# Optimization experiments

Hardware: AMD Instinct MI355X
Metric: run time of the kernel (lower is better)

Reference implementation:

```python
import jax, jax.numpy as jnp
import numpy as np

B, C, D, H, W = 2, 180, 16, 32, 32
NH, WS, I = 6, 8, 2
HD = C // NH
SCALE = HD ** -0.5
N = WS ** 3                      # 512 tokens per window
TABLE = (2 * WS - 1) ** 3        # 3375 relative-position entries
HID = int(C * 4.0)               # MLP hidden
CR = C // 3                      # CAB compressed channels (compress_ratio=3)
SQ = C // 30                     # channel-attn squeeze (squeeze_factor=30)
CONV_SCALE = 0.01
EPS = 1e-5


def layer_norm(x, g, b):
    m = jnp.mean(x, axis=-1, keepdims=True)
    v = jnp.mean((x - m) ** 2, axis=-1, keepdims=True)
    return (x - m) * jax.lax.rsqrt(v + EPS) * g + b


def setup_inputs() -> dict:
    key = jax.random.key(0)
    ks = jax.random.split(key, 12)
    n = lambda i, shape: jax.random.normal(ks[i], shape, jnp.float32) * 0.02
    return {
        "x": jax.random.normal(ks[0], (B, D * H * W, C), jnp.float32),
        "x_size_d": D, "x_size_h": H, "x_size_w": W,
        "rpi_sa": jax.random.randint(ks[1], (N, N), 0, TABLE),
        "attn_mask": jnp.zeros((1,), jnp.float32),
        "triangular_masks": jnp.zeros((1,), jnp.float32),
        "g1": jnp.ones((C,), jnp.float32), "b1": jnp.zeros((C,), jnp.float32),
        "qkv_w": n(2, (3 * C, C)), "qkv_b": jnp.zeros((3 * C,), jnp.float32),
        "rpb": n(3, (TABLE, NH)),
        "proj_w": n(4, (C, C)), "proj_b": jnp.zeros((C,), jnp.float32),
        "cw1": n(5, (CR, C, 3, 3, 3)), "cb1": jnp.zeros((CR,), jnp.float32),
        "cw2": n(6, (C, CR, 3, 3, 3)), "cb2": jnp.zeros((C,), jnp.float32),
        "caw1": n(7, (SQ, C)), "cab1": jnp.zeros((SQ,), jnp.float32),
        "caw2": n(8, (C, SQ)), "cab2": jnp.zeros((C,), jnp.float32),
        "g2": jnp.ones((C,), jnp.float32), "b2": jnp.zeros((C,), jnp.float32),
        "fc1_w": n(9, (HID, C)), "fc1_b": jnp.zeros((HID,), jnp.float32),
        "fc2_w": n(10, (C, HID)), "fc2_b": jnp.zeros((C,), jnp.float32),
    }


def reference(x, x_size_d, x_size_h, x_size_w, rpi_sa, attn_mask, triangular_masks,
              g1, b1, qkv_w, qkv_b, rpb, proj_w, proj_b,
              cw1, cb1, cw2, cb2, caw1, cab1, caw2, cab2,
              g2, b2, fc1_w, fc1_b, fc2_w, fc2_b):
    Dd, Hd, Wd = x_size_d, x_size_h, x_size_w
    shortcut = x
    xn = layer_norm(x, g1, b1).reshape(B, Dd, Hd, Wd, C)

    # ---- CAB conv branch (conv3 -> gelu -> conv3 -> channel attention) ----
    xc = jnp.transpose(xn, (0, 4, 1, 2, 3))  # B C D H W
    dn = ("NCDHW", "OIDHW", "NCDHW")
    y = jax.lax.conv_general_dilated(xc, cw1, (1, 1, 1), "SAME", dimension_numbers=dn)
    y = jax.nn.gelu(y + cb1[None, :, None, None, None], approximate=False)
    y = jax.lax.conv_general_dilated(y, cw2, (1, 1, 1), "SAME", dimension_numbers=dn)
    y = y + cb2[None, :, None, None, None]
    pooled = jnp.mean(y, axis=(2, 3, 4))                      # B C (AdaptiveAvgPool3d(1))
    a = jax.nn.relu(pooled @ caw1.T + cab1)
    a = jax.nn.sigmoid(a @ caw2.T + cab2)                     # B C
    y = y * a[:, :, None, None, None]
    conv_x = jnp.transpose(y, (0, 2, 3, 4, 1)).reshape(B, Dd * Hd * Wd, C)

    # ---- sparse interval partition (interval=2, no pad, no shift) ----
    Gd, Gh, Gw = Dd // I, Hd // I, Wd // I
    xs = xn.reshape(B, Gd, I, Gh, I, Gw, I, C)
    xs = jnp.transpose(xs, (0, 2, 4, 6, 1, 3, 5, 7)).reshape(B * I ** 3, Gd, Gh, Gw, C)

    # ---- 3D window partition ----
    nd, nh, nw = Gd // WS, Gh // WS, Gw // WS
    xw = xs.reshape(-1, nd, WS, nh, WS, nw, WS, C)
    xw = jnp.transpose(xw, (0, 1, 3, 5, 2, 4, 6, 7)).reshape(-1, N, C)

    # ---- window attention with relative-position bias ----
    qkv = (xw @ qkv_w.T + qkv_b).reshape(-1, N, 3, NH, HD)
    qkv = jnp.transpose(qkv, (2, 0, 3, 1, 4))                 # 3, nWin, NH, N, HD
    q, k, v = qkv[0] * SCALE, qkv[1], qkv[2]
    attn = jnp.einsum("whnd,whmd->whnm", q, k)
    bias = rpb[rpi_sa.reshape(-1)].reshape(N, N, NH)
    attn = jax.nn.softmax(attn + jnp.transpose(bias, (2, 0, 1))[None], axis=-1)
    out = jnp.einsum("whnm,whmd->whnd", attn, v)
    out = jnp.transpose(out, (0, 2, 1, 3)).reshape(-1, N, C)
    out = out @ proj_w.T + proj_b

    # ---- window reverse + sparse reverse ----
    xs = out.reshape(-1, nd, nh, nw, WS, WS, WS, C)
    xs = jnp.transpose(xs, (0, 1, 4, 2, 5, 3, 6, 7)).reshape(B * I ** 3, Gd, Gh, Gw, C)
    xs = xs.reshape(B, I, I, I, Gd, Gh, Gw, C)
    xs = jnp.transpose(xs, (0, 4, 1, 5, 2, 6, 3, 7)).reshape(B, Dd, Hd, Wd, C)
    attn_x = xs.reshape(B, Dd * Hd * Wd, C)

    # ---- residual + conv branch, then MLP ----
    x = shortcut + attn_x + conv_x * CONV_SCALE
    h = layer_norm(x, g2, b2)
    h = jax.nn.gelu(h @ fc1_w.T + fc1_b, approximate=False) @ fc2_w.T + fc2_b
    return x + h
```

## Files before the change

kernel.cpp:

```cpp
#include <hip/hip_runtime.h>
#include <math.h>

static constexpr int CCH = 180;
static constexpr float SCALE_Q = 0.18257418583505536f;

typedef short short8 __attribute__((ext_vector_type(8)));
typedef float f32x4 __attribute__((ext_vector_type(4)));

static constexpr size_t OFF_ATTNB = 0;
static constexpr size_t OFF_XNB   = 3145728;
static constexpr size_t OFF_Y1B   = 6291456;
static constexpr size_t OFF_QKVB  = 7340032;
static constexpr size_t OFF_HID   = 0;
static constexpr size_t OFF_Y2B   = 16777216;
static constexpr size_t OFF_X2    = 19922944;
static constexpr size_t OFF_X2N   = 25821184;
static constexpr size_t OFF_BIASB = 28966912;
static constexpr size_t OFF_WQKV  = 29753344;
static constexpr size_t OFF_WPROJ = 29814784;
static constexpr size_t OFF_WFC1  = 29839360;
static constexpr size_t OFF_WFC2  = 29913088;
static constexpr size_t OFF_WB1   = 30011392;
static constexpr size_t OFF_WB2   = 30177280;
static constexpr size_t OFF_PPART = 30343168;
static constexpr size_t OFF_POOL  = 30354688;
static constexpr size_t OFF_AM    = 30355048;

__device__ __forceinline__ float geluf(float v){
  return 0.5f*v*(1.0f + erff(v*0.70710678118654752440f));
}
__device__ __forceinline__ short f2bf(float f){
  unsigned u = __float_as_uint(f);
  unsigned r = (u + 0x7FFFu + ((u>>16)&1u)) >> 16;
  return (short)r;
}
__device__ __forceinline__ float bf2f(short s){
  return __uint_as_float(((unsigned)(unsigned short)s)<<16);
}
__device__ __forceinline__ void gload16(const void* g, void* l){
  __builtin_amdgcn_global_load_lds(
    (const __attribute__((address_space(1))) unsigned int*)g,
    (__attribute__((address_space(3))) unsigned int*)l, 16, 0, 0);
}

__global__ void prep_wb(const float* __restrict__ qkv_w, const float* __restrict__ proj_w,
                        const float* __restrict__ fc1_w, const float* __restrict__ fc2_w,
                        short* __restrict__ wq, short* __restrict__ wp,
                        short* __restrict__ w1, short* __restrict__ w2){
  int i = blockIdx.x*256 + threadIdx.x;
  if(i < 122880){
    int o = i/192, k = i - o*192;
    wq[i] = (o<540 && k<180) ? f2bf(qkv_w[o*180+k]) : (short)0;
  } else if(i < 172032){
    int j = i-122880; int o = j/192, k = j - o*192;
    wp[j] = (o<180 && k<180) ? f2bf(proj_w[o*180+k]) : (short)0;
  } else if(i < 319488){
    int j = i-172032; int o = j/192, k = j - o*192;
    w1[j] = (o<720 && k<180) ? f2bf(fc1_w[o*180+k]) : (short)0;
  } else if(i < 516096){
    int j = i-319488; int o = j/768, k = j - o*768;
    w2[j] = (o<180 && k<720) ? f2bf(fc2_w[o*720+k]) : (short)0;
  }
}

__global__ void prep_wbc(const float* __restrict__ cw1, const float* __restrict__ cw2,
                         short* __restrict__ wb1, short* __restrict__ wb2){
  int i = blockIdx.x*256 + threadIdx.x;
  if(i < 27*64*192){
    int t = i/(64*192); int rem = i - t*64*192;
    int co = rem/192, ci = rem - co*192;
    wb1[i] = (co<60 && ci<180) ? f2bf(cw1[(co*180+ci)*27 + t]) : (short)0;
    int co2 = rem/64, ci2 = rem - co2*64;
    wb2[i] = (co2<180 && ci2<60) ? f2bf(cw2[(co2*60+ci2)*27 + t]) : (short)0;
  }
}

__global__ __launch_bounds__(256) void bias_prep(const int* __restrict__ rpi,
    const float* __restrict__ rpb, short* __restrict__ biasB){
  int i = blockIdx.x*256 + threadIdx.x;
  int q = i>>9, k = i&511;
  int kt = k>>5, kin = k&31;
  int j = kt*32 + ((kin<16) ? 2*kin : 2*(kin-16)+1);
  int idx = rpi[i];
  #pragma unroll
  for(int h=0;h<6;h++)
    biasB[((size_t)h*512 + q)*512 + j] = f2bf(rpb[idx*6+h]);
}

__global__ __launch_bounds__(256) void ln_bf16(const float* __restrict__ x,
    const float* __restrict__ g, const float* __restrict__ b, short* __restrict__ outb){
  int token = blockIdx.x*4 + (threadIdx.x>>6);
  int lane  = threadIdx.x & 63;
  const float* row = x + (size_t)token*CCH;
  float v0 = row[lane], v1 = row[lane+64];
  float v2 = (lane<52) ? row[lane+128] : 0.f;
  float s = v0+v1+v2;
  #pragma unroll
  for(int m=1;m<64;m<<=1) s += __shfl_xor(s, m, 64);
  float mean = s*(1.f/180.f);
  float d0=v0-mean, d1=v1-mean, d2=(lane<52)?(v2-mean):0.f;
  float sq = d0*d0+d1*d1+d2*d2;
  #pragma unroll
  for(int m=1;m<64;m<<=1) sq += __shfl_xor(sq, m, 64);
  float rstd = rsqrtf(sq*(1.f/180.f)+1e-5f);
  short* o = outb + (size_t)token*192;
  o[lane]    = f2bf(d0*rstd*g[lane]    + b[lane]);
  o[lane+64] = f2bf(d1*rstd*g[lane+64] + b[lane+64]);
  o[lane+128]= (lane<52) ? f2bf(d2*rstd*g[lane+128] + b[lane+128]) : (short)0;
}

__global__ __launch_bounds__(256) void conv1_mfma(const short* __restrict__ in,
    const short* __restrict__ wb, const float* __restrict__ cbias, short* __restrict__ y1b){
  __shared__ short lds[136*192];
  int bid = blockIdx.x;
  int xcd = bid&7, idx = bid>>3;
  int b = idx>>5, dd = (idx>>4)&1, hg = idx&15;
  int d = xcd*2+dd;
  int h0 = hg*2;
  int tid = threadIdx.x, l=tid&63, l15=l&15, g=l>>4, wid=tid>>6;
  int hrow = wid&1, coh = wid>>1;
  f32x4 acc[2][2];
  #pragma unroll
  for(int mi=0;mi<2;mi++)
    #pragma unroll
    for(int nj=0;nj<2;nj++) acc[mi][nj]=(f32x4){0.f,0.f,0.f,0.f};
  short8 stg[13];

  auto LOADS = [&](int kd){
    int dp = d+kd-1;
    bool dok = (unsigned)dp<16u;
    const short* src = in + ((size_t)(b*16 + (dok?dp:0))*1024)*192;
    #pragma unroll
    for(int it=0; it<13; it++){
      if(it<12 || tid<192){
        int idx2 = tid + it*256;
        int rr = idx2/24, s = idx2 - rr*24;
        int hl = rr/34, wl = rr - hl*34;
        int hh = h0 - 1 + hl, w = wl - 1;
        short8 v = (short8){0,0,0,0,0,0,0,0};
        if(dok && (unsigned)hh<32u && (unsigned)w<32u)
          v = *(const short8*)&src[((size_t)hh*32+w)*192 + s*8];
        stg[it] = v;
      }
    }
  };
  auto WRITES = [&](){
    #pragma unroll
    for(int it=0; it<13; it++){
      if(it<12 || tid<192){
        int idx2 = tid + it*256;
        int rr = idx2/24, s = idx2 - rr*24;
        *(short8*)&lds[rr*192 + (((s&~7)|((s&7)^(rr&7)))<<3)] = stg[it];
      }
    }
  };
  LOADS(0); WRITES(); __syncthreads();
  for(int kd=0; kd<3; kd++){
    if(kd<2) LOADS(kd+1);
    #pragma unroll
    for(int kh=0;kh<3;kh++)
    #pragma unroll
    for(int kw=0;kw<3;kw++){
      const short* wt = wb + (size_t)((kd*3+kh)*3+kw)*12288;
      #pragma unroll
      for(int ks=0;ks<6;ks++){
        int s = ks*4+g;
        short8 av[2], bv[2];
        #pragma unroll
        for(int mi=0;mi<2;mi++){
          int rr = (hrow+kh)*34 + kw + mi*16 + l15;
          av[mi] = *(const short8*)&lds[rr*192 + (((s&~7)|((s&7)^(rr&7)))<<3)];
        }
        #pragma unroll
        for(int nj=0;nj<2;nj++)
          bv[nj] = *(const short8*)&wt[(size_t)(coh*32+nj*16+l15)*192 + ks*32 + g*8];
        #pragma unroll
        for(int mi=0;mi<2;mi++)
          #pragma unroll
          for(int nj=0;nj<2;nj++)
            acc[mi][nj] = __builtin_amdgcn_mfma_f32_16x16x32_bf16(av[mi], bv[nj], acc[mi][nj],0,0,0);
      }
    }
    __syncthreads();
    if(kd<2){ WRITES(); __syncthreads(); }
  }
  size_t token0 = ((size_t)(b*16+d)*32 + h0)*32;
  #pragma unroll
  for(int mi=0;mi<2;mi++)
    #pragma unroll
    for(int nj=0;nj<2;nj++){
      int co = coh*32 + nj*16 + l15;
      float bb = (co<60)? cbias[co] : 0.f;
      #pragma unroll
      for(int reg=0;reg<4;reg++){
        int r = hrow*32 + mi*16 + g*4 + reg;
        y1b[(token0 + r)*64 + co] = f2bf(geluf(acc[mi][nj][reg] + bb));
      }
    }
}

__global__ __launch_bounds__(512) void conv2_mfma(const short* __restrict__ in,
    const short* __restrict__ wb, const float* __restrict__ cbias, short* __restrict__ y2b){
  __shared__ short lds[136*64];
  int bid = blockIdx.x;
  int xcd = bid&7, idx = bid>>3;
  int b = idx>>5, dd = (idx>>4)&1, hg = idx&15;
  int d = xcd*2+dd;
  int h0 = hg*2;
  int tid = threadIdx.x, l=tid&63, l15=l&15, g=l>>4, wid=tid>>6;
  int hrow = wid&1, coq = wid>>1;
  f32x4 acc[2][3];
  #pragma unroll
  for(int mi=0;mi<2;mi++)
    #pragma unroll
    for(int nj=0;nj<3;nj++) acc[mi][nj]=(f32x4){0.f,0.f,0.f,0.f};
  short8 stg[3];

  auto LOADS = [&](int kd){
    int dp = d+kd-1;
    bool dok = (unsigned)dp<16u;
    const short* src = in + ((size_t)(b*16 + (dok?dp:0))*1024)*64;
    #pragma unroll
    for(int it=0; it<3; it++){
      if(it<2 || tid<64){
        int idx2 = tid + it*512;
        int rr = idx2>>3, s = idx2&7;
        int hl = rr/34, wl = rr - hl*34;
        int hh = h0 - 1 + hl, w = wl - 1;
        short8 v = (short8){0,0,0,0,0,0,0,0};
        if(dok && (unsigned)hh<32u && (unsigned)w<32u)
          v = *(const short8*)&src[((size_t)hh*32+w)*64 + s*8];
        stg[it] = v;
      }
    }
  };
  auto WRITES = [&](){
    #pragma unroll
    for(int it=0; it<3; it++){
      if(it<2 || tid<64){
        int idx2 = tid + it*512;
        int rr = idx2>>3, s = idx2&7;
        *(short8*)&lds[rr*64 + ((s^(rr&7))<<3)] = stg[it];
      }
    }
  };
  LOADS(0); WRITES(); __syncthreads();
  for(int kd=0; kd<3; kd++){
    if(kd<2) LOADS(kd+1);
    #pragma unroll
    for(int kh=0;kh<3;kh++)
    #pragma unroll
    for(int kw=0;kw<3;kw++){
      const short* wt = wb + (size_t)((kd*3+kh)*3+kw)*12288;
      #pragma unroll
      for(int ks=0;ks<2;ks++){
        int s = ks*4+g;
        short8 av[2], bv[3];
        #pragma unroll
        for(int mi=0;mi<2;mi++){
          int rr = (hrow+kh)*34 + kw + mi*16 + l15;
          av[mi] = *(const short8*)&lds[rr*64 + ((s^(rr&7))<<3)];
        }
        #pragma unroll
        for(int nj=0;nj<3;nj++)
          bv[nj] = *(const short8*)&wt[(size_t)(coq*48+nj*16+l15)*64 + ks*32 + g*8];
        #pragma unroll
        for(int mi=0;mi<2;mi++)
          #pragma unroll
          for(int nj=0;nj<3;nj++)
            acc[mi][nj] = __builtin_amdgcn_mfma_f32_16x16x32_bf16(av[mi], bv[nj], acc[mi][nj],0,0,0);
      }
    }
    __syncthreads();
    if(kd<2){ WRITES(); __syncthreads(); }
  }
  size_t token0 = ((size_t)(b*16+d)*32 + h0)*32;
  #pragma unroll
  for(int mi=0;mi<2;mi++)
    #pragma unroll
    for(int nj=0;nj<3;nj++){
      int co = coq*48 + nj*16 + l15;
      float bb = (co<180)? cbias[co] : 0.f;
      #pragma unroll
      for(int reg=0;reg<4;reg++){
        int r = hrow*32 + mi*16 + g*4 + reg;
        y2b[(token0 + r)*192 + co] = f2bf(acc[mi][nj][reg] + bb);
      }
    }
}

__global__ __launch_bounds__(192) void pool1_kernel(const short* __restrict__ y2b,
                                                    float* __restrict__ part){
  int b = blockIdx.x>>5, chunk = blockIdx.x&31;
  int c = threadIdx.x;
  if(c<180){
    float s = 0.f;
    const short* base = y2b + ((size_t)b*16384 + chunk*512)*192 + c;
    for(int it=0;it<512;it++) s += bf2f(base[(size_t)it*192]);
    part[blockIdx.x*180 + c] = s;
  }
}
__global__ void pool2_kernel(const float* __restrict__ part, float* __restrict__ pooled){
  int i = blockIdx.x*256 + threadIdx.x;
  if(i<360){
    int b = i/180, c = i - b*180;
    float s = 0.f;
    for(int ch=0;ch<32;ch++) s += part[(b*32+ch)*180 + c];
    pooled[i] = s*(1.f/16384.f);
  }
}

__global__ void chattn_kernel(const float* __restrict__ pooled,
    const float* __restrict__ caw1, const float* __restrict__ cab1,
    const float* __restrict__ caw2, const float* __restrict__ cab2,
    float* __restrict__ amask){
  __shared__ float hid[2][6];
  int t = threadIdx.x;
  if(t<12){
    int b = t/6, qh = t - b*6;
    float s = cab1[qh];
    for(int c=0;c<180;c++) s += pooled[b*180+c]*caw1[qh*180+c];
    hid[b][qh] = fmaxf(s, 0.f);
  }
  __syncthreads();
  for(int i=t;i<360;i+=64){
    int b = i/180, c = i - b*180;
    float s = cab2[c];
    #pragma unroll
    for(int qh=0;qh<6;qh++) s += hid[b][qh]*caw2[c*6+qh];
    amask[i] = 1.f/(1.f+__expf(-s));
  }
}

__device__ __forceinline__ int wtok_to_row(int t){
  int win = t >> 9, n = t & 511;
  int sb = win >> 2, wi = win & 3;
  int wh = wi >> 1, ww = wi & 1;
  int b  = sb >> 3, r = sb & 7;
  int id = r >> 2, ih = (r>>1)&1, iw = r&1;
  int td = n >> 6, th = (n>>3)&7, tw = n & 7;
  int dd = td*2 + id;
  int hh = (wh*8+th)*2 + ih;
  int wwp= (ww*8+tw)*2 + iw;
  return b*16384 + (dd*32+hh)*32 + wwp;
}

template<int MODE, int NOUT, int KTOT>
__global__ __launch_bounds__(256) void mgemm(const short* __restrict__ A,
    const short* __restrict__ Wb, const float* __restrict__ bias, void* __restrict__ outv,
    const float* __restrict__ e0, const float* __restrict__ e1,
    const float* __restrict__ e2){
  __shared__ short As[2][8192];
  __shared__ short Bs[2][8192];
  __shared__ int rowmap[128];
  int lin = blockIdx.y*gridDim.x + blockIdx.x;
  int xcd = lin&7, k = lin>>3;
  int bm = xcd*32 + (k & 31);
  int bn = k >> 5;
  int tid = threadIdx.x;
  int l = tid&63, l15=l&15, g=l>>4, wid=tid>>6;
  int wm = wid>>1, wn = wid&1;
  constexpr int RS = (MODE==3)?768:192;
  if(MODE==0 || MODE==1){
    if(tid<128) rowmap[tid] = wtok_to_row(bm*128+tid);
  }
  __syncthreads();
  f32x4 acc[4][4];
  #pragma unroll
  for(int i=0;i<4;i++)
    #pragma unroll
    for(int j=0;j<4;j++) acc[i][j] = (f32x4){0.f,0.f,0.f,0.f};

  constexpr int NCH = KTOT/64;
  auto STAGE = [&](int ch, int p){
    int k0 = ch*64;
    #pragma unroll
    for(int it=0; it<4; it++){
      int i = it*256 + wid*64 + l;
      int r = i>>3, sl = (i&7) ^ (r&7);
      size_t row = (MODE==0) ? (size_t)rowmap[r] : (size_t)(bm*128+r);
      gload16(A + row*RS + k0 + sl*8, &As[p][(size_t)(it*256+wid*64)*8]);
    }
    #pragma unroll
    for(int it=0; it<4; it++){
      int i = it*256 + wid*64 + l;
      int c = i>>3, sl = (i&7) ^ (c&7);
      gload16(Wb + (size_t)(bn*128+c)*KTOT + k0 + sl*8, &Bs[p][(size_t)(it*256+wid*64)*8]);
    }
  };
  STAGE(0,0);
  for(int ch=0; ch<NCH; ch++){
    if(ch+1<NCH){
      STAGE(ch+1,(ch+1)&1);
      asm volatile("s_waitcnt vmcnt(8)" ::: "memory");
    } else {
      asm volatile("s_waitcnt vmcnt(0)" ::: "memory");
    }
    __builtin_amdgcn_s_barrier();
    const short* as = As[ch&1];
    const short* bs = Bs[ch&1];
    #pragma unroll
    for(int ks=0; ks<2; ks++){
      short8 av[4], bv[4];
      #pragma unroll
      for(int i=0;i<4;i++){
        int r = wm*64 + i*16 + l15;
        av[i] = *(const short8*)&as[r*64 + (((ks*4+g) ^ (r&7))<<3)];
      }
      #pragma unroll
      for(int j=0;j<4;j++){
        int c = wn*64 + j*16 + l15;
        bv[j] = *(const short8*)&bs[c*64 + (((ks*4+g) ^ (c&7))<<3)];
      }
      #pragma unroll
      for(int i=0;i<4;i++)
        #pragma unroll
        for(int j=0;j<4;j++)
          acc[i][j] = __builtin_amdgcn_mfma_f32_16x16x32_bf16(av[i], bv[j], acc[i][j],0,0,0);
    }
    asm volatile("" ::: "memory");
    __builtin_amdgcn_s_barrier();
  }
  #pragma unroll
  for(int i=0;i<4;i++){
    int rloc0 = wm*64 + i*16 + g*4;
    #pragma unroll
    for(int j=0;j<4;j++){
      int o = bn*128 + wn*64 + j*16 + l15;
      if(MODE!=2 && o>=NOUT) continue;
      float bb = (o<NOUT) ? bias[o] : 0.f;
      #pragma unroll
      for(int reg=0; reg<4; reg++){
        int rl = rloc0 + reg;
        int trow = bm*128 + rl;
        float v = acc[i][j][reg] + bb;
        if(MODE==0){
          int which = o/180; int chn = o - which*180;
          int head = chn/30; int hd = chn - head*30;
          int win = trow>>9, n = trow&511;
          if(which==0){
            size_t sidx = ((size_t)(win*6+head)*512 + n)*32;
            ((short*)outv)[sidx + hd] = f2bf(v*SCALE_Q);
            if(hd==0) *(int*)&((short*)outv)[sidx + 30] = 0;
          } else if(which==1){
            size_t sidx = 6291456 + ((size_t)(win*6+head)*512 + n)*32;
            ((short*)outv)[sidx + hd] = f2bf(v);
            if(hd==0) *(int*)&((short*)outv)[sidx + 30] = 0;
          } else {
            ((short*)outv)[12582912 + ((size_t)(win*6+head)*32 + hd)*512 + n] = f2bf(v);
          }
        } else if(MODE==1){
          int grow = rowmap[rl];
          float conv = bf2f(((const short*)e1)[(size_t)grow*192 + o]);
          float am   = e2[(grow>>14)*180 + o];
          ((float*)outv)[(size_t)grow*180+o] = v + e0[(size_t)grow*180+o] + conv*am*0.01f;
        } else if(MODE==2){
          ((short*)outv)[(size_t)trow*768+o] = (o<720) ? f2bf(geluf(v)) : (short)0;
        } else {
          ((float*)outv)[(size_t)trow*180+o] = v + e0[(size_t)trow*180+o];
        }
      }
    }
  }
}

__global__ __launch_bounds__(256) void attn_mfma(const short* __restrict__ qkvb,
    const short* __restrict__ biasB, short* __restrict__ attnb){
  __shared__ short Ks[1024];
  __shared__ short Vt[1024];
  __shared__ short Ps[4096];
  int bid = blockIdx.x;
  int j0 = bid>>3;
  int grp = (bid&7)*48 + (j0>>2);
  int qt = j0&3;
  int win = grp/6, head = grp - (grp/6)*6;
  int tid = threadIdx.x, w = tid>>6, l = tid&63, l15 = l&15, g = l>>4;
  const short* qp = qkvb + (size_t)(win*6+head)*16384;
  const short* kp = qp + 6291456;
  const short* vp = qkvb + 12582912 + (size_t)(win*6+head)*16384;
  int qbase = qt*128 + w*32;
  short8 aq0 = *(const short8*)&qp[(size_t)(qbase + l15)*32 + g*8];
  short8 aq1 = *(const short8*)&qp[(size_t)(qbase + 16 + l15)*32 + g*8];
  const short* bB = biasB + ((size_t)head*512 + qbase)*512;
  f32x4 acc[2][2];
  float lsum[2][4];
  #pragma unroll
  for(int a=0;a<2;a++){
    #pragma unroll
    for(int r=0;r<4;r++) lsum[a][r]=0.f;
    #pragma unroll
    for(int b=0;b<2;b++) acc[a][b]=(f32x4){0.f,0.f,0.f,0.f};
  }
  int pbase = w*1024;
  int rrA = l15>>1, sA = ((l15&1)<<2)|g;
  int offT0 = rrA*64 + ((sA ^ (rrA&7))<<3);
  int rrB = 8+rrA;
  int offT1 = rrB*64 + ((sA ^ (rrB&7))<<3);
  int strr = (tid&127)>>3, sts = tid&7;
  int stoff = strr*64 + ((sts ^ (strr&7))<<3);
  int sttok = strr*2 + (sts>>2), sthd8 = (sts&3)*8;

  for(int kt=0; kt<16; kt++){
    if(tid<128){
      short8 v = *(const short8*)&kp[(size_t)(kt*32+sttok)*32 + sthd8];
      *(short8*)&Ks[stoff] = v;
    } else {
      short8 v = *(const short8*)&vp[(size_t)sttok*512 + kt*32 + sthd8];
      *(short8*)&Vt[stoff] = v;
    }
    unsigned ub[2][4];
    #pragma unroll
    for(int mf=0; mf<2; mf++)
      #pragma unroll
      for(int reg=0; reg<4; reg++)
        ub[mf][reg] = *(const unsigned*)&bB[(size_t)(mf*16+g*4+reg)*512 + kt*32 + 2*l15];
    __syncthreads();
    short8 bk0 = *(const short8*)&Ks[offT0];
    short8 bk1 = *(const short8*)&Ks[offT1];
    f32x4 z = (f32x4){0.f,0.f,0.f,0.f};
    f32x4 s00 = __builtin_amdgcn_mfma_f32_16x16x32_bf16(aq0, bk0, z,0,0,0);
    f32x4 s01 = __builtin_amdgcn_mfma_f32_16x16x32_bf16(aq0, bk1, z,0,0,0);
    f32x4 s10 = __builtin_amdgcn_mfma_f32_16x16x32_bf16(aq1, bk0, z,0,0,0);
    f32x4 s11 = __builtin_amdgcn_mfma_f32_16x16x32_bf16(aq1, bk1, z,0,0,0);
    #pragma unroll
    for(int mf=0; mf<2; mf++){
      #pragma unroll
      for(int reg=0; reg<4; reg++){
        float b0 = __uint_as_float(ub[mf][reg]<<16);
        float b1 = __uint_as_float(ub[mf][reg]&0xFFFF0000u);
        float sv0 = (mf==0)? s00[reg] : s10[reg];
        float sv1 = (mf==0)? s01[reg] : s11[reg];
        float p0 = __expf(fminf(sv0 + b0, 60.f));
        float p1 = __expf(fminf(sv1 + b1, 60.f));
        lsum[mf][reg] += p0 + p1;
        int q = mf*16 + g*4 + reg;
        int rr = q>>1;
        int s0 = ((q&1)<<2) | (l15>>3);
        int s1 = s0 + 2;
        Ps[pbase + rr*64 + ((s0 ^ (rr&7))<<3) + (l15&7)] = f2bf(p0);
        Ps[pbase + rr*64 + ((s1 ^ (rr&7))<<3) + (l15&7)] = f2bf(p1);
      }
    }
    short8 ap0 = *(const short8*)&Ps[pbase + offT0];
    short8 ap1 = *(const short8*)&Ps[pbase + offT1];
    short8 bv0 = *(const short8*)&Vt[offT0];
    short8 bv1 = *(const short8*)&Vt[offT1];
    acc[0][0] = __builtin_amdgcn_mfma_f32_16x16x32_bf16(ap0, bv0, acc[0][0],0,0,0);
    acc[0][1] = __builtin_amdgcn_mfma_f32_16x16x32_bf16(ap0, bv1, acc[0][1],0,0,0);
    acc[1][0] = __builtin_amdgcn_mfma_f32_16x16x32_bf16(ap1, bv0, acc[1][0],0,0,0);
    acc[1][1] = __builtin_amdgcn_mfma_f32_16x16x32_bf16(ap1, bv1, acc[1][1],0,0,0);
    __syncthreads();
  }
  int token = win*512 + qbase;
  #pragma unroll
  for(int mf=0; mf<2; mf++)
  #pragma unroll
  for(int reg=0; reg<4; reg++){
    float lv = lsum[mf][reg];
    lv += __shfl_xor(lv,1,64); lv += __shfl_xor(lv,2,64);
    lv += __shfl_xor(lv,4,64); lv += __shfl_xor(lv,8,64);
    float inv = 1.f/lv;
    int qg = token + mf*16 + g*4 + reg;
    short* orow = attnb + (size_t)qg*192 + head*30;
    if(l15<30) orow[l15] = f2bf(acc[mf][0][reg]*inv);
    if(l15<14) orow[16+l15] = f2bf(acc[mf][1][reg]*inv);
    if(head==5 && l15<12) attnb[(size_t)qg*192 + 180 + l15] = 0;
  }
}

extern "C" void kernel_launch(void* const* d_in, const int* in_sizes, int n_in,
                              void* d_out, int out_size, void* d_ws, size_t ws_size,
                              hipStream_t stream){
  const float* x      = (const float*)d_in[0];
  const int*   rpi    = (const int*)  d_in[4];
  const float* g1     = (const float*)d_in[7];
  const float* b1     = (const float*)d_in[8];
  const float* qkv_w  = (const float*)d_in[9];
  const float* qkv_b  = (const float*)d_in[10];
  const float* rpb    = (const float*)d_in[11];
  const float* proj_w = (const float*)d_in[12];
  const float* proj_b = (const float*)d_in[13];
  const float* cw1    = (const float*)d_in[14];
  const float* cb1    = (const float*)d_in[15];
  const float* cw2    = (const float*)d_in[16];
  const float* cb2    = (const float*)d_in[17];
  const float* caw1   = (const float*)d_in[18];
  const float* cab1   = (const float*)d_in[19];
  const float* caw2   = (const float*)d_in[20];
  const float* cab2   = (const float*)d_in[21];
  const float* g2     = (const float*)d_in[22];
  const float* b2     = (const float*)d_in[23];
  const float* fc1_w  = (const float*)d_in[24];
  const float* fc1_b  = (const float*)d_in[25];
  const float* fc2_w  = (const float*)d_in[26];
  const float* fc2_b  = (const float*)d_in[27];
  float* ws = (float*)d_ws;
  float* fout = (float*)d_out;
  short* attnb = (short*)(ws + OFF_ATTNB);
  short* xnb   = (short*)(ws + OFF_XNB);
  short* y1b   = (short*)(ws + OFF_Y1B);
  short* qkvb  = (short*)(ws + OFF_QKVB);
  short* hid   = (short*)(ws + OFF_HID);
  short* y2b   = (short*)(ws + OFF_Y2B);
  short* x2n   = (short*)(ws + OFF_X2N);
  short* biasB = (short*)(ws + OFF_BIASB);
  short* wq    = (short*)(ws + OFF_WQKV);
  short* wp    = (short*)(ws + OFF_WPROJ);
  short* w1    = (short*)(ws + OFF_WFC1);
  short* w2    = (short*)(ws + OFF_WFC2);
  short* wb1   = (short*)(ws + OFF_WB1);
  short* wb2   = (short*)(ws + OFF_WB2);

  prep_wb<<<2016,256,0,stream>>>(qkv_w, proj_w, fc1_w, fc2_w, wq, wp, w1, w2);
  prep_wbc<<<1296,256,0,stream>>>(cw1, cw2, wb1, wb2);
  bias_prep<<<1024,256,0,stream>>>(rpi, rpb, biasB);
  ln_bf16<<<8192,256,0,stream>>>(x, g1, b1, xnb);
  conv1_mfma<<<512,256,0,stream>>>(xnb, wb1, cb1, y1b);
  conv2_mfma<<<512,512,0,stream>>>(y1b, wb2, cb2, y2b);
  pool1_kernel<<<64,192,0,stream>>>(y2b, ws+OFF_PPART);
  pool2_kernel<<<2,256,0,stream>>>(ws+OFF_PPART, ws+OFF_POOL);
  chattn_kernel<<<1,64,0,stream>>>(ws+OFF_POOL, caw1, cab1, caw2, cab2, ws+OFF_AM);
  mgemm<0,540,192><<<dim3(256,5),256,0,stream>>>(
      xnb, wq, qkv_b, qkvb, nullptr, nullptr, nullptr);
  attn_mfma<<<1536,256,0,stream>>>(qkvb, biasB, attnb);
  mgemm<1,180,192><<<dim3(256,2),256,0,stream>>>(
      attnb, wp, proj_b, ws+OFF_X2, x, (const float*)y2b, ws+OFF_AM);
  ln_bf16<<<8192,256,0,stream>>>(ws+OFF_X2, g2, b2, x2n);
  mgemm<2,720,192><<<dim3(256,6),256,0,stream>>>(
      x2n, w1, fc1_b, hid, nullptr, nullptr, nullptr);
  mgemm<3,180,768><<<dim3(256,2),256,0,stream>>>(
      hid, w2, fc2_b, fout, ws+OFF_X2, nullptr, nullptr);
}
```

Before: 499.8 us.

## Use zero-padded activation layouts so conv kernels stage halos with direct LDS loads

```diff
diff --git a/kernel.cpp b/kernel.cpp
--- a/kernel.cpp
+++ b/kernel.cpp
@@ -8,23 +8,23 @@
 typedef float f32x4 __attribute__((ext_vector_type(4)));
 
 static constexpr size_t OFF_ATTNB = 0;
-static constexpr size_t OFF_XNB   = 3145728;
-static constexpr size_t OFF_Y1B   = 6291456;
-static constexpr size_t OFF_QKVB  = 7340032;
+static constexpr size_t OFF_XNP   = 3145728;
+static constexpr size_t OFF_Y1P   = 7140864;
+static constexpr size_t OFF_QKVB  = 8472576;
 static constexpr size_t OFF_HID   = 0;
-static constexpr size_t OFF_Y2B   = 16777216;
-static constexpr size_t OFF_X2    = 19922944;
-static constexpr size_t OFF_X2N   = 25821184;
-static constexpr size_t OFF_BIASB = 28966912;
-static constexpr size_t OFF_WQKV  = 29753344;
-static constexpr size_t OFF_WPROJ = 29814784;
-static constexpr size_t OFF_WFC1  = 29839360;
-static constexpr size_t OFF_WFC2  = 29913088;
-static constexpr size_t OFF_WB1   = 30011392;
-static constexpr size_t OFF_WB2   = 30177280;
-static constexpr size_t OFF_PPART = 30343168;
-static constexpr size_t OFF_POOL  = 30354688;
-static constexpr size_t OFF_AM    = 30355048;
+static constexpr size_t OFF_Y2B   = 17909760;
+static constexpr size_t OFF_X2    = 21055488;
+static constexpr size_t OFF_X2N   = 26953728;
+static constexpr size_t OFF_BIASB = 30099456;
+static constexpr size_t OFF_WQKV  = 30885888;
+static constexpr size_t OFF_WPROJ = 30947328;
+static constexpr size_t OFF_WFC1  = 30971904;
+static constexpr size_t OFF_WFC2  = 31045632;
+static constexpr size_t OFF_WB1   = 31143936;
+static constexpr size_t OFF_WB2   = 31309824;
+static constexpr size_t OFF_PPART = 31475712;
+static constexpr size_t OFF_POOL  = 31487232;
+static constexpr size_t OFF_AM    = 31487592;
 
 __device__ __forceinline__ float geluf(float v){
   return 0.5f*v*(1.0f + erff(v*0.70710678118654752440f));
@@ -87,6 +87,7 @@
     biasB[((size_t)h*512 + q)*512 + j] = f2bf(rpb[idx*6+h]);
 }
 
+template<int PADDED>
 __global__ __launch_bounds__(256) void ln_bf16(const float* __restrict__ x,
     const float* __restrict__ g, const float* __restrict__ b, short* __restrict__ outb){
   int token = blockIdx.x*4 + (threadIdx.x>>6);
@@ -103,188 +104,149 @@
   #pragma unroll
   for(int m=1;m<64;m<<=1) sq += __shfl_xor(sq, m, 64);
   float rstd = rsqrtf(sq*(1.f/180.f)+1e-5f);
-  short* o = outb + (size_t)token*192;
+  size_t orow;
+  if(PADDED){
+    int bb=token>>14, d=(token>>10)&15, h=(token>>5)&31, w=token&31;
+    orow = ((size_t)((bb*18+d+1)*34 + h+1)*34 + w+1)*192;
+  } else {
+    orow = (size_t)token*192;
+  }
+  short* o = outb + orow;
   o[lane]    = f2bf(d0*rstd*g[lane]    + b[lane]);
   o[lane+64] = f2bf(d1*rstd*g[lane+64] + b[lane+64]);
   o[lane+128]= (lane<52) ? f2bf(d2*rstd*g[lane+128] + b[lane+128]) : (short)0;
 }
 
-__global__ __launch_bounds__(256) void conv1_mfma(const short* __restrict__ in,
-    const short* __restrict__ wb, const float* __restrict__ cbias, short* __restrict__ y1b){
-  __shared__ short lds[136*192];
+__global__ __launch_bounds__(256,2) void conv1_mfma(const short* __restrict__ in,
+    const short* __restrict__ wb, const float* __restrict__ cbias, short* __restrict__ y1p){
+  __shared__ short lds[2][19584];
   int bid = blockIdx.x;
   int xcd = bid&7, idx = bid>>3;
-  int b = idx>>5, dd = (idx>>4)&1, hg = idx&15;
+  int b = idx>>6, dd=(idx>>5)&1, h=idx&31;
   int d = xcd*2+dd;
-  int h0 = hg*2;
-  int tid = threadIdx.x, l=tid&63, l15=l&15, g=l>>4, wid=tid>>6;
-  int hrow = wid&1, coh = wid>>1;
-  f32x4 acc[2][2];
+  int tid=threadIdx.x, l=tid&63, l15=l&15, g=l>>4, wid=tid>>6;
+  int soff[10];
+  #pragma unroll
+  for(int it=0; it<10; it++){
+    int i = it*256 + tid;
+    int rr = i/24, s = i - rr*24;
+    soff[it] = rr*192 + (((s&~7)|((s&7)^(rr&7)))<<3);
+  }
+  f32x4 acc[2];
+  acc[0]=(f32x4){0.f,0.f,0.f,0.f}; acc[1]=(f32x4){0.f,0.f,0.f,0.f};
+  auto STAGE=[&](int kd,int p){
+    const short* S = in + ((size_t)((b*18+d+kd)*34 + h)*34)*192;
+    #pragma unroll
+    for(int it=0; it<10; it++){
+      if(it<9 || tid<144)
+        gload16(S + soff[it], &lds[p][(it*256 + wid*64)*8]);
+    }
+  };
+  STAGE(0,0);
+  __syncthreads();
+  for(int kd=0;kd<3;kd++){
+    if(kd<2) STAGE(kd+1,(kd+1)&1);
+    const short* buf = lds[kd&1];
+    #pragma unroll
+    for(int kh=0;kh<3;kh++)
+    #pragma unroll
+    for(int kw=0;kw<3;kw++){
+      const short* wt = wb + (size_t)((kd*3+kh)*3+kw)*12288 + (wid*16+l15)*192;
+      int rr0 = kh*34+kw+l15, rr1 = rr0+16;
+      #pragma unroll
+      for(int ks=0;ks<6;ks++){
+        int s = ks*4+g;
+        short8 a0 = *(const short8*)&buf[rr0*192 + (((s&~7)|((s&7)^(rr0&7)))<<3)];
+        short8 a1 = *(const short8*)&buf[rr1*192 + (((s&~7)|((s&7)^(rr1&7)))<<3)];
+        short8 bv = *(const short8*)&wt[ks*32 + g*8];
+        acc[0] = __builtin_amdgcn_mfma_f32_16x16x32_bf16(a0, bv, acc[0],0,0,0);
+        acc[1] = __builtin_amdgcn_mfma_f32_16x16x32_bf16(a1, bv, acc[1],0,0,0);
+      }
+    }
+    __syncthreads();
+  }
+  int co = wid*16+l15;
+  float bb = (co<60)? cbias[co] : 0.f;
+  size_t row0 = ((size_t)(b*18+d+1)*34 + h+1)*34 + 1;
   #pragma unroll
   for(int mi=0;mi<2;mi++)
     #pragma unroll
-    for(int nj=0;nj<2;nj++) acc[mi][nj]=(f32x4){0.f,0.f,0.f,0.f};
-  short8 stg[13];
-
-  auto LOADS = [&](int kd){
-    int dp = d+kd-1;
-    bool dok = (unsigned)dp<16u;
-    const short* src = in + ((size_t)(b*16 + (dok?dp:0))*1024)*192;
-    #pragma unroll
-    for(int it=0; it<13; it++){
-      if(it<12 || tid<192){
-        int idx2 = tid + it*256;
-        int rr = idx2/24, s = idx2 - rr*24;
-        int hl = rr/34, wl = rr - hl*34;
-        int hh = h0 - 1 + hl, w = wl - 1;
-        short8 v = (short8){0,0,0,0,0,0,0,0};
-        if(dok && (unsigned)hh<32u && (unsigned)w<32u)
-          v = *(const short8*)&src[((size_t)hh*32+w)*192 + s*8];
-        stg[it] = v;
-      }
+    for(int reg=0;reg<4;reg++){
+      int r = mi*16 + g*4 + reg;
+      y1p[(row0 + r)*64 + co] = f2bf(geluf(acc[mi][reg] + bb));
+    }
+}
+
+__global__ __launch_bounds__(256,4) void conv2_mfma(const short* __restrict__ in,
+    const short* __restrict__ wb, const float* __restrict__ cbias, short* __restrict__ y2b){
+  __shared__ short lds[2][6528];
+  int bid = blockIdx.x;
+  int xcd = bid&7, idx = bid>>3;
+  int b = idx>>6, dd=(idx>>5)&1, h=idx&31;
+  int d = xcd*2+dd;
+  int tid=threadIdx.x, l=tid&63, l15=l&15, g=l>>4, wid=tid>>6;
+  int soff[4];
+  #pragma unroll
+  for(int it=0; it<4; it++){
+    int i = it*256 + tid;
+    int rr = i>>3, s = i&7;
+    soff[it] = rr*64 + ((s^(rr&7))<<3);
+  }
+  f32x4 acc[2][3];
+  #pragma unroll
+  for(int mi=0;mi<2;mi++)
+    #pragma unroll
+    for(int nj=0;nj<3;nj++) acc[mi][nj]=(f32x4){0.f,0.f,0.f,0.f};
+  auto STAGE=[&](int kd,int p){
+    const short* S = in + ((size_t)((b*18+d+kd)*34 + h)*34)*64;
+    #pragma unroll
+    for(int it=0; it<4; it++){
+      if(it<3 || tid<48)
+        gload16(S + soff[it], &lds[p][(it*256 + wid*64)*8]);
     }
   };
-  auto WRITES = [&](){
-    #pragma unroll
-    for(int it=0; it<13; it++){
-      if(it<12 || tid<192){
-        int idx2 = tid + it*256;
-        int rr = idx2/24, s = idx2 - rr*24;
-        *(short8*)&lds[rr*192 + (((s&~7)|((s&7)^(rr&7)))<<3)] = stg[it];
-      }
-    }
-  };
-  LOADS(0); WRITES(); __syncthreads();
-  for(int kd=0; kd<3; kd++){
-    if(kd<2) LOADS(kd+1);
+  STAGE(0,0);
+  __syncthreads();
+  for(int kd=0;kd<3;kd++){
+    if(kd<2) STAGE(kd+1,(kd+1)&1);
+    const short* buf = lds[kd&1];
     #pragma unroll
     for(int kh=0;kh<3;kh++)
     #pragma unroll
     for(int kw=0;kw<3;kw++){
       const short* wt = wb + (size_t)((kd*3+kh)*3+kw)*12288;
-      #pragma unroll
-      for(int ks=0;ks<6;ks++){
-        int s = ks*4+g;
-        short8 av[2], bv[2];
-        #pragma unroll
-        for(int mi=0;mi<2;mi++){
-          int rr = (hrow+kh)*34 + kw + mi*16 + l15;
-          av[mi] = *(const short8*)&lds[rr*192 + (((s&~7)|((s&7)^(rr&7)))<<3)];
-        }
-        #pragma unroll
-        for(int nj=0;nj<2;nj++)
-          bv[nj] = *(const short8*)&wt[(size_t)(coh*32+nj*16+l15)*192 + ks*32 + g*8];
-        #pragma unroll
-        for(int mi=0;mi<2;mi++)
-          #pragma unroll
-          for(int nj=0;nj<2;nj++)
-            acc[mi][nj] = __builtin_amdgcn_mfma_f32_16x16x32_bf16(av[mi], bv[nj], acc[mi][nj],0,0,0);
-      }
-    }
-    __syncthreads();
-    if(kd<2){ WRITES(); __syncthreads(); }
-  }
-  size_t token0 = ((size_t)(b*16+d)*32 + h0)*32;
-  #pragma unroll
-  for(int mi=0;mi<2;mi++)
-    #pragma unroll
-    for(int nj=0;nj<2;nj++){
-      int co = coh*32 + nj*16 + l15;
-      float bb = (co<60)? cbias[co] : 0.f;
-      #pragma unroll
-      for(int reg=0;reg<4;reg++){
-        int r = hrow*32 + mi*16 + g*4 + reg;
-        y1b[(token0 + r)*64 + co] = f2bf(geluf(acc[mi][nj][reg] + bb));
-      }
-    }
-}
-
-__global__ __launch_bounds__(512) void conv2_mfma(const short* __restrict__ in,
-    const short* __restrict__ wb, const float* __restrict__ cbias, short* __restrict__ y2b){
-  __shared__ short lds[136*64];
-  int bid = blockIdx.x;
-  int xcd = bid&7, idx = bid>>3;
-  int b = idx>>5, dd = (idx>>4)&1, hg = idx&15;
-  int d = xcd*2+dd;
-  int h0 = hg*2;
-  int tid = threadIdx.x, l=tid&63, l15=l&15, g=l>>4, wid=tid>>6;
-  int hrow = wid&1, coq = wid>>1;
-  f32x4 acc[2][3];
-  #pragma unroll
-  for(int mi=0;mi<2;mi++)
-    #pragma unroll
-    for(int nj=0;nj<3;nj++) acc[mi][nj]=(f32x4){0.f,0.f,0.f,0.f};
-  short8 stg[3];
-
-  auto LOADS = [&](int kd){
-    int dp = d+kd-1;
-    bool dok = (unsigned)dp<16u;
-    const short* src = in + ((size_t)(b*16 + (dok?dp:0))*1024)*64;
-    #pragma unroll
-    for(int it=0; it<3; it++){
-      if(it<2 || tid<64){
-        int idx2 = tid + it*512;
-        int rr = idx2>>3, s = idx2&7;
-        int hl = rr/34, wl = rr - hl*34;
-        int hh = h0 - 1 + hl, w = wl - 1;
-        short8 v = (short8){0,0,0,0,0,0,0,0};
-        if(dok && (unsigned)hh<32u && (unsigned)w<32u)
-          v = *(const short8*)&src[((size_t)hh*32+w)*64 + s*8];
-        stg[it] = v;
-      }
-    }
-  };
-  auto WRITES = [&](){
-    #pragma unroll
-    for(int it=0; it<3; it++){
-      if(it<2 || tid<64){
-        int idx2 = tid + it*512;
-        int rr = idx2>>3, s = idx2&7;
-        *(short8*)&lds[rr*64 + ((s^(rr&7))<<3)] = stg[it];
-      }
-    }
-  };
-  LOADS(0); WRITES(); __syncthreads();
-  for(int kd=0; kd<3; kd++){
-    if(kd<2) LOADS(kd+1);
-    #pragma unroll
-    for(int kh=0;kh<3;kh++)
-    #pragma unroll
-    for(int kw=0;kw<3;kw++){
-      const short* wt = wb + (size_t)((kd*3+kh)*3+kw)*12288;
+      int rr0 = kh*34+kw+l15, rr1 = rr0+16;
       #pragma unroll
       for(int ks=0;ks<2;ks++){
         int s = ks*4+g;
-        short8 av[2], bv[3];
-        #pragma unroll
-        for(int mi=0;mi<2;mi++){
-          int rr = (hrow+kh)*34 + kw + mi*16 + l15;
-          av[mi] = *(const short8*)&lds[rr*64 + ((s^(rr&7))<<3)];
-        }
+        short8 a0 = *(const short8*)&buf[rr0*64 + ((s^(rr0&7))<<3)];
+        short8 a1 = *(const short8*)&buf[rr1*64 + ((s^(rr1&7))<<3)];
+        short8 bv[3];
         #pragma unroll
         for(int nj=0;nj<3;nj++)
-          bv[nj] = *(const short8*)&wt[(size_t)(coq*48+nj*16+l15)*64 + ks*32 + g*8];
+          bv[nj] = *(const short8*)&wt[(size_t)(wid*48+nj*16+l15)*64 + ks*32 + g*8];
         #pragma unroll
-        for(int mi=0;mi<2;mi++)
-          #pragma unroll
-          for(int nj=0;nj<3;nj++)
-            acc[mi][nj] = __builtin_amdgcn_mfma_f32_16x16x32_bf16(av[mi], bv[nj], acc[mi][nj],0,0,0);
+        for(int nj=0;nj<3;nj++){
+          acc[0][nj] = __builtin_amdgcn_mfma_f32_16x16x32_bf16(a0, bv[nj], acc[0][nj],0,0,0);
+          acc[1][nj] = __builtin_amdgcn_mfma_f32_16x16x32_bf16(a1, bv[nj], acc[1][nj],0,0,0);
+        }
       }
     }
     __syncthreads();
-    if(kd<2){ WRITES(); __syncthreads(); }
-  }
-  size_t token0 = ((size_t)(b*16+d)*32 + h0)*32;
+  }
+  size_t token0 = ((size_t)(b*16+d)*32 + h)*32;
   #pragma unroll
   for(int mi=0;mi<2;mi++)
     #pragma unroll
     for(int nj=0;nj<3;nj++){
-      int co = coq*48 + nj*16 + l15;
-      float bb = (co<180)? cbias[co] : 0.f;
-      #pragma unroll
-      for(int reg=0;reg<4;reg++){
-        int r = hrow*32 + mi*16 + g*4 + reg;
-        y2b[(token0 + r)*192 + co] = f2bf(acc[mi][nj][reg] + bb);
+      int co = wid*48 + nj*16 + l15;
+      if(co<180){
+        float bb = cbias[co];
+        #pragma unroll
+        for(int reg=0;reg<4;reg++){
+          int r = mi*16 + g*4 + reg;
+          y2b[(token0 + r)*192 + co] = f2bf(acc[mi][nj][reg] + bb);
+        }
       }
     }
 }
@@ -332,17 +294,24 @@
   }
 }
 
-__device__ __forceinline__ int wtok_to_row(int t){
+__device__ __forceinline__ void wtok_decomp(int t, int& b, int& dd, int& hh, int& ww){
   int win = t >> 9, n = t & 511;
   int sb = win >> 2, wi = win & 3;
-  int wh = wi >> 1, ww = wi & 1;
-  int b  = sb >> 3, r = sb & 7;
+  int wh = wi >> 1, wwi = wi & 1;
+  b = sb >> 3; int r = sb & 7;
   int id = r >> 2, ih = (r>>1)&1, iw = r&1;
   int td = n >> 6, th = (n>>3)&7, tw = n & 7;
-  int dd = td*2 + id;
-  int hh = (wh*8+th)*2 + ih;
-  int wwp= (ww*8+tw)*2 + iw;
-  return b*16384 + (dd*32+hh)*32 + wwp;
+  dd = td*2 + id;
+  hh = (wh*8+th)*2 + ih;
+  ww = (wwi*8+tw)*2 + iw;
+}
+__device__ __forceinline__ int wtok_to_row(int t){
+  int b,dd,hh,ww; wtok_decomp(t,b,dd,hh,ww);
+  return b*16384 + (dd*32+hh)*32 + ww;
+}
+__device__ __forceinline__ int wtok_to_prow(int t){
+  int b,dd,hh,ww; wtok_decomp(t,b,dd,hh,ww);
+  return ((b*18+dd+1)*34 + hh+1)*34 + ww + 1;
 }
 
 template<int MODE, int NOUT, int KTOT>
@@ -362,7 +331,7 @@
   int wm = wid>>1, wn = wid&1;
   constexpr int RS = (MODE==3)?768:192;
   if(MODE==0 || MODE==1){
-    if(tid<128) rowmap[tid] = wtok_to_row(bm*128+tid);
+    if(tid<128) rowmap[tid] = (MODE==0) ? wtok_to_prow(bm*128+tid) : wtok_to_row(bm*128+tid);
   }
   __syncthreads();
   f32x4 acc[4][4];
@@ -378,7 +347,7 @@
     for(int it=0; it<4; it++){
       int i = it*256 + wid*64 + l;
       int r = i>>3, sl = (i&7) ^ (r&7);
-      size_t row = (MODE==0) ? (size_t)rowmap[r] : (size_t)(bm*128+r);
+      size_t row = (size_t)((MODE==0||MODE==1) ? rowmap[r] : bm*128+r);
       gload16(A + row*RS + k0 + sl*8, &As[p][(size_t)(it*256+wid*64)*8]);
     }
     #pragma unroll
@@ -489,7 +458,7 @@
     #pragma unroll
     for(int r=0;r<4;r++) lsum[a][r]=0.f;
     #pragma unroll
-    for(int b=0;b<2;b++) acc[a][b]=(f32x4){0.f,0.f,0.f,0.f};
+    for(int b2=0;b2<2;b2++) acc[a][b2]=(f32x4){0.f,0.f,0.f,0.f};
   }
   int pbase = w*1024;
   int rrA = l15>>1, sA = ((l15&1)<<2)|g;
@@ -597,8 +566,8 @@
   float* ws = (float*)d_ws;
   float* fout = (float*)d_out;
   short* attnb = (short*)(ws + OFF_ATTNB);
-  short* xnb   = (short*)(ws + OFF_XNB);
-  short* y1b   = (short*)(ws + OFF_Y1B);
+  short* xnp   = (short*)(ws + OFF_XNP);
+  short* y1p   = (short*)(ws + OFF_Y1P);
   short* qkvb  = (short*)(ws + OFF_QKVB);
   short* hid   = (short*)(ws + OFF_HID);
   short* y2b   = (short*)(ws + OFF_Y2B);
@@ -611,21 +580,23 @@
   short* wb1   = (short*)(ws + OFF_WB1);
   short* wb2   = (short*)(ws + OFF_WB2);
 
+  hipMemsetAsync(xnp, 0, (size_t)7990272*2, stream);
+  hipMemsetAsync(y1p, 0, (size_t)2663424*2, stream);
   prep_wb<<<2016,256,0,stream>>>(qkv_w, proj_w, fc1_w, fc2_w, wq, wp, w1, w2);
   prep_wbc<<<1296,256,0,stream>>>(cw1, cw2, wb1, wb2);
   bias_prep<<<1024,256,0,stream>>>(rpi, rpb, biasB);
-  ln_bf16<<<8192,256,0,stream>>>(x, g1, b1, xnb);
-  conv1_mfma<<<512,256,0,stream>>>(xnb, wb1, cb1, y1b);
-  conv2_mfma<<<512,512,0,stream>>>(y1b, wb2, cb2, y2b);
+  ln_bf16<1><<<8192,256,0,stream>>>(x, g1, b1, xnp);
+  conv1_mfma<<<1024,256,0,stream>>>(xnp, wb1, cb1, y1p);
+  conv2_mfma<<<1024,256,0,stream>>>(y1p, wb2, cb2, y2b);
   pool1_kernel<<<64,192,0,stream>>>(y2b, ws+OFF_PPART);
   pool2_kernel<<<2,256,0,stream>>>(ws+OFF_PPART, ws+OFF_POOL);
   chattn_kernel<<<1,64,0,stream>>>(ws+OFF_POOL, caw1, cab1, caw2, cab2, ws+OFF_AM);
   mgemm<0,540,192><<<dim3(256,5),256,0,stream>>>(
-      xnb, wq, qkv_b, qkvb, nullptr, nullptr, nullptr);
+      xnp, wq, qkv_b, qkvb, nullptr, nullptr, nullptr);
   attn_mfma<<<1536,256,0,stream>>>(qkvb, biasB, attnb);
   mgemm<1,180,192><<<dim3(256,2),256,0,stream>>>(
       attnb, wp, proj_b, ws+OFF_X2, x, (const float*)y2b, ws+OFF_AM);
-  ln_bf16<<<8192,256,0,stream>>>(ws+OFF_X2, g2, b2, x2n);
+  ln_bf16<0><<<8192,256,0,stream>>>(ws+OFF_X2, g2, b2, x2n);
   mgemm<2,720,192><<<dim3(256,6),256,0,stream>>>(
       x2n, w1, fc1_b, hid, nullptr, nullptr, nullptr);
   mgemm<3,180,768><<<dim3(256,2),256,0,stream>>>(
```

Result: slower. 638.2 us (+27.7%).
